# Kernel tuning notes

Hardware: AMD Instinct MI355X
Metric: run time of the kernel (lower is better)

The kernel has to match this reference:

```python
import jax, jax.numpy as jnp
import numpy as np

D_MODEL = 1024
D_K = 64  # d_model // heads


def setup_inputs() -> dict:
    key = jax.random.key(0)
    ks = jax.random.split(key, 9)
    B, S = 8, 2048
    q = jax.random.normal(ks[0], (B, S, D_MODEL), dtype=jnp.float32)
    k = jax.random.normal(ks[1], (B, S, D_MODEL), dtype=jnp.float32)
    v = jax.random.normal(ks[2], (B, S, D_MODEL), dtype=jnp.float32)
    # Causal mask: True = blocked (masked_fill with -inf)
    mask = ~jnp.tril(jnp.ones((S, S), dtype=bool))
    # Linear params (stored as [in, out]); torch Linear init ~ U(-1/sqrt(in), 1/sqrt(in))
    lim = 1.0 / np.sqrt(D_MODEL)
    Wq = jax.random.uniform(ks[3], (D_MODEL, D_K), jnp.float32, -lim, lim)
    Wk = jax.random.uniform(ks[4], (D_MODEL, D_K), jnp.float32, -lim, lim)
    Wv = jax.random.uniform(ks[5], (D_MODEL, D_K), jnp.float32, -lim, lim)
    bq = jax.random.uniform(ks[6], (D_K,), jnp.float32, -lim, lim)
    bk = jax.random.uniform(ks[7], (D_K,), jnp.float32, -lim, lim)
    bv = jax.random.uniform(ks[8], (D_K,), jnp.float32, -lim, lim)
    return {"q": q, "k": k, "v": v, "mask": mask,
            "Wq": Wq, "bq": bq, "Wk": Wk, "bk": bk, "Wv": Wv, "bv": bv}


def reference(q, k, v, mask, Wq, bq, Wk, bk, Wv, bv):
    qp = q @ Wq + bq              # [B, S, d_k]
    kp = k @ Wk + bk              # [B, S, d_k]
    vp = v @ Wv + bv              # [B, S, d_k]
    scale = 1.0 / jnp.sqrt(jnp.float32(D_K))
    scores = jnp.einsum("bqd,bkd->bqk", qp, kp) * scale  # [B, S, S]
    scores = jnp.where(mask, -jnp.inf, scores)
    attn = jax.nn.softmax(scores, axis=-1)
    return jnp.einsum("bqk,bkd->bqd", attn, vp)  # [B, S, d_k]
```

## Files before the change

### kernel.cpp

```cpp
#include <hip/hip_runtime.h>
#include <hip/hip_bf16.h>

typedef short s4 __attribute__((ext_vector_type(4)));
typedef short s8 __attribute__((ext_vector_type(8)));
typedef float f4 __attribute__((ext_vector_type(4)));

#define MFMA16(a, b, c) __builtin_amdgcn_mfma_f32_16x16x16bf16_1k(a, b, c, 0, 0, 0)

__device__ __forceinline__ short f2bf(float f) {
    union { float f; unsigned u; } v; v.f = f;
    unsigned r = v.u + 0x7fffu + ((v.u >> 16) & 1u);
    return (short)(r >> 16);
}

struct ProjArgs {
    const float* X[3];
    const float* W[3];
    const float* b[3];
    unsigned short* O[3];
};

__global__ __launch_bounds__(256) void proj_kernel(ProjArgs args) {
    __shared__ short lA[64][68];
    __shared__ short lW[64][68];

    const int t  = threadIdx.x;
    const int wv = t >> 6, ln = t & 63, lg = ln >> 4, lr = ln & 15;
    const int which = blockIdx.y;

    const float* X = args.X[which] + (size_t)blockIdx.x * 64 * 1024;
    const float* W = args.W[which];

    f4 acc[4] = {f4{0,0,0,0}, f4{0,0,0,0}, f4{0,0,0,0}, f4{0,0,0,0}};

    for (int kk = 0; kk < 1024; kk += 64) {
        #pragma unroll
        for (int i = 0; i < 4; ++i) {
            int f  = t + i * 256;
            int r  = f >> 4;
            int c4 = f & 15;
            f4 a = *(const f4*)(X + (size_t)r * 1024 + kk + c4 * 4);
            f4 w = *(const f4*)(W + (size_t)(kk + r) * 64 + c4 * 4);
            s4 ab; ab[0]=f2bf(a[0]); ab[1]=f2bf(a[1]); ab[2]=f2bf(a[2]); ab[3]=f2bf(a[3]);
            s4 wb; wb[0]=f2bf(w[0]); wb[1]=f2bf(w[1]); wb[2]=f2bf(w[2]); wb[3]=f2bf(w[3]);
            *(s4*)&lA[r][c4 * 4] = ab;
            *(s4*)&lW[r][c4 * 4] = wb;
        }
        __syncthreads();

        #pragma unroll
        for (int ks = 0; ks < 4; ++ks) {
            s4 af = *(const s4*)&lA[wv * 16 + lr][ks * 16 + 4 * lg];
            #pragma unroll
            for (int nf = 0; nf < 4; ++nf) {
                s4 bf;
                #pragma unroll
                for (int e = 0; e < 4; ++e)
                    bf[e] = lW[ks * 16 + 4 * lg + e][nf * 16 + lr];
                acc[nf] = MFMA16(af, bf, acc[nf]);
            }
        }
        __syncthreads();
    }

    const float* bias = args.b[which];
    unsigned short* O = args.O[which];
    #pragma unroll
    for (int nf = 0; nf < 4; ++nf) {
        float bs = bias[nf * 16 + lr];
        int col = nf * 16 + lr;
        #pragma unroll
        for (int e = 0; e < 4; ++e) {
            int r = wv * 16 + 4 * lg + e;
            int grow = blockIdx.x * 64 + r;
            unsigned short val = (unsigned short)f2bf(acc[nf][e] + bs);
            if (which == 2) {
                size_t idx = (size_t)(grow >> 11) * 131072
                           + (size_t)((grow & 2047) >> 6) * 4096
                           + (size_t)col * 64 + (grow & 63);
                O[idx] = val;
            } else {
                O[(size_t)grow * 64 + col] = val;
            }
        }
    }
}

__global__ __launch_bounds__(512) void attn_part(const unsigned short* __restrict__ qp,
                                                 const unsigned short* __restrict__ kp,
                                                 const unsigned short* __restrict__ vpT,
                                                 float* __restrict__ partO,
                                                 float* __restrict__ partML) {
    __shared__ short lK[2][2][64][72];
    __shared__ short lV[2][2][64][72];

    const int t    = threadIdx.x;
    const int wave = t >> 6, ln = t & 63, lg = ln >> 4, lr = ln & 15;
    const int half = wave >> 2, hw = wave & 3;
    const int b = blockIdx.y, x = blockIdx.x;
    const int qt = 31 - (x >> 1), z = x & 1;
    const int P = qt + 1;
    const int c = (P + 1) >> 1;
    const int base  = z ? c : 0;
    const int chunk = z ? (P - c) : c;
    const int hA = (chunk + 1) >> 1;
    const int qrow = qt * 64 + hw * 16 + lr;

    const int g = t >> 7, gi = t & 127, ghalf = g >> 1;
    const bool isV = (g & 1) != 0;
    const unsigned short* tb = (isV ? vpT : kp) + (size_t)b * 131072;

    const unsigned short* qpb = qp + (size_t)b * 131072;
    s4 qf[4];
    #pragma unroll
    for (int ks = 0; ks < 4; ++ks)
        qf[ks] = *(const s4*)(qpb + (size_t)qrow * 64 + ks * 16 + 4 * lg);

    f4 accO[4] = {f4{0,0,0,0}, f4{0,0,0,0}, f4{0,0,0,0}, f4{0,0,0,0}};
    float m = -3e38f, lsum = 0.f;

    s8 stg[4];
    {
        const unsigned short* p = tb + (size_t)(base + (ghalf ? hA : 0)) * 4096;
        #pragma unroll
        for (int i = 0; i < 4; ++i)
            stg[i] = *(const s8*)(p + (gi + 128 * i) * 8);
    }

    int buf = 0;
    for (int j = 0; j < hA; ++j) {
        {
            short (*dst)[72] = isV ? lV[ghalf][buf] : lK[ghalf][buf];
            #pragma unroll
            for (int i = 0; i < 4; ++i) {
                int s = gi + 128 * i;
                *(s8*)&dst[s >> 3][(s & 7) * 8] = stg[i];
            }
        }
        __syncthreads();

        if (j + 1 < hA) {
            const unsigned short* p = tb + (size_t)(base + (ghalf ? hA : 0) + j + 1) * 4096;
            #pragma unroll
            for (int i = 0; i < 4; ++i)
                stg[i] = *(const s8*)(p + (gi + 128 * i) * 8);
        }

        const int kt = base + (half ? hA : 0) + j;
        if (kt < base + chunk) {
            f4 st[4];
            #pragma unroll
            for (int kf = 0; kf < 4; ++kf) {
                f4 a = f4{0,0,0,0};
                #pragma unroll
                for (int ks = 0; ks < 4; ++ks) {
                    s4 kfr = *(const s4*)&lK[half][buf][kf * 16 + lr][ks * 16 + 4 * lg];
                    a = MFMA16(kfr, qf[ks], a);
                }
                st[kf] = a;
            }

            const bool diag = (kt == qt);
            const int kbase = kt * 64;
            float smax = -3e38f;
            #pragma unroll
            for (int kf = 0; kf < 4; ++kf) {
                #pragma unroll
                for (int e = 0; e < 4; ++e) {
                    float s = st[kf][e] * 0.125f;
                    if (diag && (kbase + kf * 16 + 4 * lg + e > qrow)) s = -3e38f;
                    st[kf][e] = s;
                    smax = fmaxf(smax, s);
                }
            }
            smax = fmaxf(smax, __shfl_xor(smax, 16));
            smax = fmaxf(smax, __shfl_xor(smax, 32));

            float mnew  = fmaxf(m, smax);
            float scale = __expf(m - mnew);
            float psum  = 0.f;
            s4 pf[4];
            #pragma unroll
            for (int kf = 0; kf < 4; ++kf) {
                f4 p;
                #pragma unroll
                for (int e = 0; e < 4; ++e) { p[e] = __expf(st[kf][e] - mnew); psum += p[e]; }
                s4 pb; pb[0]=f2bf(p[0]); pb[1]=f2bf(p[1]); pb[2]=f2bf(p[2]); pb[3]=f2bf(p[3]);
                pf[kf] = pb;
            }
            psum += __shfl_xor(psum, 16);
            psum += __shfl_xor(psum, 32);
            lsum = lsum * scale + psum;
            m = mnew;
            #pragma unroll
            for (int df = 0; df < 4; ++df) accO[df] *= scale;

            #pragma unroll
            for (int df = 0; df < 4; ++df) {
                #pragma unroll
                for (int kf = 0; kf < 4; ++kf) {
                    s4 vf = *(const s4*)&lV[half][buf][df * 16 + lr][kf * 16 + 4 * lg];
                    accO[df] = MFMA16(vf, pf[kf], accO[df]);
                }
            }
        }
        buf ^= 1;
    }

    __syncthreads();
    float* ex = (float*)&lK[0][0][0][0];
    const int idx = (hw * 64 + ln) * 19;
    if (half == 1) {
        ex[idx + 0] = m;
        ex[idx + 1] = lsum;
        #pragma unroll
        for (int df = 0; df < 4; ++df)
            #pragma unroll
            for (int e = 0; e < 4; ++e)
                ex[idx + 2 + df * 4 + e] = accO[df][e];
    }
    __syncthreads();
    if (half == 0) {
        float mB = ex[idx + 0], lB = ex[idx + 1];
        float mx = fmaxf(m, mB);
        float sA = __expf(m - mx), sB = __expf(mB - mx);
        float lP = lsum * sA + lB * sB;

        const size_t pidx = ((size_t)b * 32 + qt) * 2 + z;
        float* Od = partO + pidx * 4096;
        const int q = hw * 16 + lr;
        #pragma unroll
        for (int df = 0; df < 4; ++df) {
            f4 o;
            #pragma unroll
            for (int e = 0; e < 4; ++e)
                o[e] = accO[df][e] * sA + ex[idx + 2 + df * 4 + e] * sB;
            *(f4*)(Od + (size_t)q * 64 + df * 16 + 4 * lg) = o;
        }
        if (lg == 0) {
            partML[pidx * 128 + q * 2 + 0] = mx;
            partML[pidx * 128 + q * 2 + 1] = lP;
        }
    }
}

__global__ __launch_bounds__(256) void attn_merge(const float* __restrict__ partO,
                                                  const float* __restrict__ partML,
                                                  float* __restrict__ out) {
    const int t = threadIdx.x;
    const int g = blockIdx.x, b = blockIdx.y;
    const int q = t >> 2, dq = t & 3;

    const size_t p0 = ((size_t)b * 32 + g) * 2;
    const size_t p1 = p0 + 1;
    float m0 = partML[p0 * 128 + q * 2], l0 = partML[p0 * 128 + q * 2 + 1];
    float m1 = partML[p1 * 128 + q * 2], l1 = partML[p1 * 128 + q * 2 + 1];
    float M  = fmaxf(m0, m1);
    float s0 = __expf(m0 - M), s1 = __expf(m1 - M);
    float inv = 1.f / (l0 * s0 + l1 * s1);

    const float* O0 = partO + p0 * 4096 + (size_t)q * 64 + dq * 16;
    const float* O1 = partO + p1 * 4096 + (size_t)q * 64 + dq * 16;
    float* ob = out + ((size_t)b * 2048 + g * 64 + q) * 64 + dq * 16;
    #pragma unroll
    for (int i = 0; i < 4; ++i) {
        f4 a = *(const f4*)(O0 + 4 * i);
        f4 c = *(const f4*)(O1 + 4 * i);
        f4 o;
        #pragma unroll
        for (int e = 0; e < 4; ++e) o[e] = (a[e] * s0 + c[e] * s1) * inv;
        *(f4*)(ob + 4 * i) = o;
    }
}

extern "C" void kernel_launch(void* const* d_in, const int* in_sizes, int n_in,
                              void* d_out, int out_size, void* d_ws, size_t ws_size,
                              hipStream_t stream) {
    const float* q  = (const float*)d_in[0];
    const float* k  = (const float*)d_in[1];
    const float* v  = (const float*)d_in[2];
    const float* Wq = (const float*)d_in[4];
    const float* bq = (const float*)d_in[5];
    const float* Wk = (const float*)d_in[6];
    const float* bk = (const float*)d_in[7];
    const float* Wv = (const float*)d_in[8];
    const float* bv = (const float*)d_in[9];

    unsigned short* qp  = (unsigned short*)d_ws;
    unsigned short* kp  = qp + (size_t)16384 * 64;
    unsigned short* vpT = kp + (size_t)16384 * 64;
    float* partO  = (float*)(vpT + (size_t)16384 * 64);
    float* partML = partO + (size_t)512 * 4096;

    ProjArgs pa;
    pa.X[0] = q;  pa.X[1] = k;  pa.X[2] = v;
    pa.W[0] = Wq; pa.W[1] = Wk; pa.W[2] = Wv;
    pa.b[0] = bq; pa.b[1] = bk; pa.b[2] = bv;
    pa.O[0] = qp; pa.O[1] = kp; pa.O[2] = vpT;
    proj_kernel<<<dim3(256, 3), 256, 0, stream>>>(pa);

    attn_part<<<dim3(64, 8), 512, 0, stream>>>(qp, kp, vpT, partO, partML);
    attn_merge<<<dim3(32, 8), 256, 0, stream>>>(partO, partML, (float*)d_out);
}
```

Before: 78.67 us.

## Use 32x32 MFMA with 128-row query tiles and pre-convert weights to bf16

Restructures the attention kernel so each block handles 128 query rows: each wave owns 32 rows and uses the 32x32x8 bf16 MFMA, which cuts LDS re-reads of K/V per query and halves the grid. Masking now applies only to tiles that intersect the diagonal, and key tiles lying entirely above a wave's rows are skipped. A separate small kernel converts the projection weights to bf16 once, so the projection kernel loads bf16 directly instead of converting W in every block. The change adds a kernel launch, alters the LDS padding and the layout of the partial buffers, and halves the number of attention blocks, which may reduce occupancy across the GPU.

```diff
diff --git a/kernel.cpp b/kernel.cpp
--- a/kernel.cpp
+++ b/kernel.cpp
@@ -4,8 +4,10 @@
 typedef short s4 __attribute__((ext_vector_type(4)));
 typedef short s8 __attribute__((ext_vector_type(8)));
 typedef float f4 __attribute__((ext_vector_type(4)));
+typedef float f16v __attribute__((ext_vector_type(16)));
 
 #define MFMA16(a, b, c) __builtin_amdgcn_mfma_f32_16x16x16bf16_1k(a, b, c, 0, 0, 0)
+#define MFMA32(a, b, c) __builtin_amdgcn_mfma_f32_32x32x8bf16_1k(a, b, c, 0, 0, 0)
 
 __device__ __forceinline__ short f2bf(float f) {
     union { float f; unsigned u; } v; v.f = f;
@@ -13,23 +15,33 @@
     return (short)(r >> 16);
 }
 
+struct WcArgs { const float* W[3]; unsigned short* O; };
+
+__global__ __launch_bounds__(256) void wconv_kernel(WcArgs a) {
+    const int which = blockIdx.y;
+    const int id = blockIdx.x * 256 + threadIdx.x;
+    f4 w = *(const f4*)(a.W[which] + (size_t)id * 4);
+    s4 o; o[0]=f2bf(w[0]); o[1]=f2bf(w[1]); o[2]=f2bf(w[2]); o[3]=f2bf(w[3]);
+    *(s4*)(a.O + (size_t)which * 65536 + (size_t)id * 4) = o;
+}
+
 struct ProjArgs {
     const float* X[3];
-    const float* W[3];
     const float* b[3];
+    const unsigned short* Wbf;
     unsigned short* O[3];
 };
 
 __global__ __launch_bounds__(256) void proj_kernel(ProjArgs args) {
     __shared__ short lA[64][68];
-    __shared__ short lW[64][68];
+    __shared__ short lW[64][72];
 
     const int t  = threadIdx.x;
     const int wv = t >> 6, ln = t & 63, lg = ln >> 4, lr = ln & 15;
     const int which = blockIdx.y;
 
     const float* X = args.X[which] + (size_t)blockIdx.x * 64 * 1024;
-    const float* W = args.W[which];
+    const unsigned short* Wb = args.Wbf + (size_t)which * 65536;
 
     f4 acc[4] = {f4{0,0,0,0}, f4{0,0,0,0}, f4{0,0,0,0}, f4{0,0,0,0}};
 
@@ -40,11 +52,15 @@
             int r  = f >> 4;
             int c4 = f & 15;
             f4 a = *(const f4*)(X + (size_t)r * 1024 + kk + c4 * 4);
-            f4 w = *(const f4*)(W + (size_t)(kk + r) * 64 + c4 * 4);
             s4 ab; ab[0]=f2bf(a[0]); ab[1]=f2bf(a[1]); ab[2]=f2bf(a[2]); ab[3]=f2bf(a[3]);
-            s4 wb; wb[0]=f2bf(w[0]); wb[1]=f2bf(w[1]); wb[2]=f2bf(w[2]); wb[3]=f2bf(w[3]);
             *(s4*)&lA[r][c4 * 4] = ab;
-            *(s4*)&lW[r][c4 * 4] = wb;
+        }
+        #pragma unroll
+        for (int i = 0; i < 2; ++i) {
+            int s = t + i * 256;
+            int r = s >> 3, c8 = s & 7;
+            s8 w8 = *(const s8*)(Wb + (size_t)(kk + r) * 64 + c8 * 8);
+            *(s8*)&lW[r][c8 * 8] = w8;
         }
         __syncthreads();
 
@@ -91,37 +107,41 @@
                                                  const unsigned short* __restrict__ vpT,
                                                  float* __restrict__ partO,
                                                  float* __restrict__ partML) {
-    __shared__ short lK[2][2][64][72];
-    __shared__ short lV[2][2][64][72];
-
-    const int t    = threadIdx.x;
-    const int wave = t >> 6, ln = t & 63, lg = ln >> 4, lr = ln & 15;
-    const int half = wave >> 2, hw = wave & 3;
+    __shared__ short lK[2][2][64][76];
+    __shared__ short lV[2][2][64][76];
+
+    const int t = threadIdx.x;
+    const int wave = t >> 6, l = t & 63, lq = l & 31, h = l >> 5;
+    const int qcol = wave >> 1, half = wave & 1;
     const int b = blockIdx.y, x = blockIdx.x;
-    const int qt = 31 - (x >> 1), z = x & 1;
-    const int P = qt + 1;
-    const int c = (P + 1) >> 1;
-    const int base  = z ? c : 0;
-    const int chunk = z ? (P - c) : c;
-    const int hA = (chunk + 1) >> 1;
-    const int qrow = qt * 64 + hw * 16 + lr;
-
-    const int g = t >> 7, gi = t & 127, ghalf = g >> 1;
-    const bool isV = (g & 1) != 0;
-    const unsigned short* tb = (isV ? vpT : kp) + (size_t)b * 131072;
+    const int g = 15 - (x >> 1), z = x & 1;
+    const int cnt = g + 1;
+    const int base = z * cnt, hA = (cnt + 1) >> 1;
+    const int qg = 128 * g + 32 * qcol + lq;
+    const int qmaxw = 128 * g + 32 * qcol + 31;
+    const int qminw = 128 * g + 32 * qcol;
+
+    const int sg = t >> 7, gi = t & 127, sHalf = sg >> 1;
+    const bool sIsV = (sg & 1) != 0;
+    const unsigned short* tb = (sIsV ? vpT : kp) + (size_t)b * 131072;
 
     const unsigned short* qpb = qp + (size_t)b * 131072;
-    s4 qf[4];
+    s4 qf[8];
     #pragma unroll
-    for (int ks = 0; ks < 4; ++ks)
-        qf[ks] = *(const s4*)(qpb + (size_t)qrow * 64 + ks * 16 + 4 * lg);
-
-    f4 accO[4] = {f4{0,0,0,0}, f4{0,0,0,0}, f4{0,0,0,0}, f4{0,0,0,0}};
+    for (int ks = 0; ks < 8; ++ks)
+        qf[ks] = *(const s4*)(qpb + (size_t)qg * 64 + ks * 8 + 4 * h);
+
+    f16v accO[2];
+    #pragma unroll
+    for (int df = 0; df < 2; ++df)
+        #pragma unroll
+        for (int r = 0; r < 16; ++r) accO[df][r] = 0.f;
     float m = -3e38f, lsum = 0.f;
 
     s8 stg[4];
     {
-        const unsigned short* p = tb + (size_t)(base + (ghalf ? hA : 0)) * 4096;
+        int tile = base + (sHalf ? hA : 0); if (tile > 31) tile = 31;
+        const unsigned short* p = tb + (size_t)tile * 4096;
         #pragma unroll
         for (int i = 0; i < 4; ++i)
             stg[i] = *(const s8*)(p + (gi + 128 * i) * 8);
@@ -130,94 +150,105 @@
     int buf = 0;
     for (int j = 0; j < hA; ++j) {
         {
-            short (*dst)[72] = isV ? lV[ghalf][buf] : lK[ghalf][buf];
+            short (*dst)[76] = sIsV ? lV[sHalf][buf] : lK[sHalf][buf];
             #pragma unroll
             for (int i = 0; i < 4; ++i) {
                 int s = gi + 128 * i;
-                *(s8*)&dst[s >> 3][(s & 7) * 8] = stg[i];
+                s4 lo = __builtin_shufflevector(stg[i], stg[i], 0, 1, 2, 3);
+                s4 hi = __builtin_shufflevector(stg[i], stg[i], 4, 5, 6, 7);
+                *(s4*)&dst[s >> 3][(s & 7) * 8] = lo;
+                *(s4*)&dst[s >> 3][(s & 7) * 8 + 4] = hi;
             }
         }
         __syncthreads();
 
         if (j + 1 < hA) {
-            const unsigned short* p = tb + (size_t)(base + (ghalf ? hA : 0) + j + 1) * 4096;
+            int tile = base + (sHalf ? hA : 0) + j + 1; if (tile > 31) tile = 31;
+            const unsigned short* p = tb + (size_t)tile * 4096;
             #pragma unroll
             for (int i = 0; i < 4; ++i)
                 stg[i] = *(const s8*)(p + (gi + 128 * i) * 8);
         }
 
         const int kt = base + (half ? hA : 0) + j;
-        if (kt < base + chunk) {
-            f4 st[4];
-            #pragma unroll
-            for (int kf = 0; kf < 4; ++kf) {
-                f4 a = f4{0,0,0,0};
-                #pragma unroll
-                for (int ks = 0; ks < 4; ++ks) {
-                    s4 kfr = *(const s4*)&lK[half][buf][kf * 16 + lr][ks * 16 + 4 * lg];
-                    a = MFMA16(kfr, qf[ks], a);
+        const int kbase = kt * 64;
+        if (kt < base + cnt && kbase <= qmaxw) {
+            f16v st[2];
+            #pragma unroll
+            for (int s = 0; s < 2; ++s)
+                #pragma unroll
+                for (int r = 0; r < 16; ++r) st[s][r] = 0.f;
+            #pragma unroll
+            for (int ks = 0; ks < 8; ++ks) {
+                s4 k0 = *(const s4*)&lK[half][buf][lq][ks * 8 + 4 * h];
+                s4 k1 = *(const s4*)&lK[half][buf][32 + lq][ks * 8 + 4 * h];
+                st[0] = MFMA32(k0, qf[ks], st[0]);
+                st[1] = MFMA32(k1, qf[ks], st[1]);
+            }
+
+            const bool needMask = (kbase + 63 > qminw);
+            float smax = -3e38f;
+            #pragma unroll
+            for (int s = 0; s < 2; ++s)
+                #pragma unroll
+                for (int r = 0; r < 16; ++r) {
+                    int key = kbase + s * 32 + 8 * (r >> 2) + 4 * h + (r & 3);
+                    float val = st[s][r] * 0.125f;
+                    if (needMask && key > qg) val = -3e38f;
+                    st[s][r] = val;
+                    smax = fmaxf(smax, val);
                 }
-                st[kf] = a;
-            }
-
-            const bool diag = (kt == qt);
-            const int kbase = kt * 64;
-            float smax = -3e38f;
-            #pragma unroll
-            for (int kf = 0; kf < 4; ++kf) {
-                #pragma unroll
-                for (int e = 0; e < 4; ++e) {
-                    float s = st[kf][e] * 0.125f;
-                    if (diag && (kbase + kf * 16 + 4 * lg + e > qrow)) s = -3e38f;
-                    st[kf][e] = s;
-                    smax = fmaxf(smax, s);
-                }
-            }
-            smax = fmaxf(smax, __shfl_xor(smax, 16));
             smax = fmaxf(smax, __shfl_xor(smax, 32));
 
             float mnew  = fmaxf(m, smax);
             float scale = __expf(m - mnew);
-            float psum  = 0.f;
-            s4 pf[4];
-            #pragma unroll
-            for (int kf = 0; kf < 4; ++kf) {
-                f4 p;
-                #pragma unroll
-                for (int e = 0; e < 4; ++e) { p[e] = __expf(st[kf][e] - mnew); psum += p[e]; }
-                s4 pb; pb[0]=f2bf(p[0]); pb[1]=f2bf(p[1]); pb[2]=f2bf(p[2]); pb[3]=f2bf(p[3]);
-                pf[kf] = pb;
-            }
-            psum += __shfl_xor(psum, 16);
+            lsum *= scale;
+            m = mnew;
+            #pragma unroll
+            for (int df = 0; df < 2; ++df)
+                #pragma unroll
+                for (int r = 0; r < 16; ++r) accO[df][r] *= scale;
+
+            float psum = 0.f;
+            #pragma unroll
+            for (int s = 0; s < 2; ++s) {
+                s4 pf[4];
+                #pragma unroll
+                for (int ks = 0; ks < 4; ++ks) {
+                    f4 p;
+                    #pragma unroll
+                    for (int e = 0; e < 4; ++e)
+                        p[e] = __expf(st[s][4 * ks + e] - mnew);
+                    psum += (p[0] + p[1]) + (p[2] + p[3]);
+                    s4 pc; pc[0]=f2bf(p[0]); pc[1]=f2bf(p[1]); pc[2]=f2bf(p[2]); pc[3]=f2bf(p[3]);
+                    pf[ks] = pc;
+                }
+                #pragma unroll
+                for (int df = 0; df < 2; ++df)
+                    #pragma unroll
+                    for (int ks = 0; ks < 4; ++ks) {
+                        s4 vf = *(const s4*)&lV[half][buf][32 * df + lq]
+                                               [s * 32 + ks * 8 + 4 * h];
+                        accO[df] = MFMA32(vf, pf[ks], accO[df]);
+                    }
+            }
             psum += __shfl_xor(psum, 32);
-            lsum = lsum * scale + psum;
-            m = mnew;
-            #pragma unroll
-            for (int df = 0; df < 4; ++df) accO[df] *= scale;
-
-            #pragma unroll
-            for (int df = 0; df < 4; ++df) {
-                #pragma unroll
-                for (int kf = 0; kf < 4; ++kf) {
-                    s4 vf = *(const s4*)&lV[half][buf][df * 16 + lr][kf * 16 + 4 * lg];
-                    accO[df] = MFMA16(vf, pf[kf], accO[df]);
-                }
-            }
+            lsum += psum;
         }
         buf ^= 1;
     }
 
     __syncthreads();
     float* ex = (float*)&lK[0][0][0][0];
-    const int idx = (hw * 64 + ln) * 19;
+    const int idx = (qcol * 64 + l) * 34;
     if (half == 1) {
         ex[idx + 0] = m;
         ex[idx + 1] = lsum;
         #pragma unroll
-        for (int df = 0; df < 4; ++df)
-            #pragma unroll
-            for (int e = 0; e < 4; ++e)
-                ex[idx + 2 + df * 4 + e] = accO[df][e];
+        for (int df = 0; df < 2; ++df)
+            #pragma unroll
+            for (int r = 0; r < 16; ++r)
+                ex[idx + 2 + df * 16 + r] = accO[df][r];
     }
     __syncthreads();
     if (half == 0) {
@@ -226,20 +257,22 @@
         float sA = __expf(m - mx), sB = __expf(mB - mx);
         float lP = lsum * sA + lB * sB;
 
-        const size_t pidx = ((size_t)b * 32 + qt) * 2 + z;
-        float* Od = partO + pidx * 4096;
-        const int q = hw * 16 + lr;
-        #pragma unroll
-        for (int df = 0; df < 4; ++df) {
-            f4 o;
-            #pragma unroll
-            for (int e = 0; e < 4; ++e)
-                o[e] = accO[df][e] * sA + ex[idx + 2 + df * 4 + e] * sB;
-            *(f4*)(Od + (size_t)q * 64 + df * 16 + 4 * lg) = o;
-        }
-        if (lg == 0) {
-            partML[pidx * 128 + q * 2 + 0] = mx;
-            partML[pidx * 128 + q * 2 + 1] = lP;
+        const size_t pidx = ((size_t)(b * 16 + g)) * 2 + z;
+        float* Od = partO + pidx * 8192 + (size_t)(32 * qcol + lq) * 64;
+        #pragma unroll
+        for (int df = 0; df < 2; ++df)
+            #pragma unroll
+            for (int rg = 0; rg < 4; ++rg) {
+                f4 o;
+                #pragma unroll
+                for (int e = 0; e < 4; ++e)
+                    o[e] = accO[df][4 * rg + e] * sA
+                         + ex[idx + 2 + df * 16 + 4 * rg + e] * sB;
+                *(f4*)(Od + 32 * df + 8 * rg + 4 * h) = o;
+            }
+        if (h == 0) {
+            partML[pidx * 256 + (32 * qcol + lq) * 2 + 0] = mx;
+            partML[pidx * 256 + (32 * qcol + lq) * 2 + 1] = lP;
         }
     }
 }
@@ -248,22 +281,22 @@
                                                   const float* __restrict__ partML,
                                                   float* __restrict__ out) {
     const int t = threadIdx.x;
-    const int g = blockIdx.x, b = blockIdx.y;
-    const int q = t >> 2, dq = t & 3;
-
-    const size_t p0 = ((size_t)b * 32 + g) * 2;
+    const int gg = blockIdx.x, b = blockIdx.y;
+    const int q = t >> 1, dh = t & 1;
+
+    const size_t p0 = ((size_t)(b * 16 + gg)) * 2;
     const size_t p1 = p0 + 1;
-    float m0 = partML[p0 * 128 + q * 2], l0 = partML[p0 * 128 + q * 2 + 1];
-    float m1 = partML[p1 * 128 + q * 2], l1 = partML[p1 * 128 + q * 2 + 1];
+    float m0 = partML[p0 * 256 + q * 2], l0 = partML[p0 * 256 + q * 2 + 1];
+    float m1 = partML[p1 * 256 + q * 2], l1 = partML[p1 * 256 + q * 2 + 1];
     float M  = fmaxf(m0, m1);
     float s0 = __expf(m0 - M), s1 = __expf(m1 - M);
     float inv = 1.f / (l0 * s0 + l1 * s1);
 
-    const float* O0 = partO + p0 * 4096 + (size_t)q * 64 + dq * 16;
-    const float* O1 = partO + p1 * 4096 + (size_t)q * 64 + dq * 16;
-    float* ob = out + ((size_t)b * 2048 + g * 64 + q) * 64 + dq * 16;
+    const float* O0 = partO + p0 * 8192 + (size_t)q * 64 + dh * 32;
+    const float* O1 = partO + p1 * 8192 + (size_t)q * 64 + dh * 32;
+    float* ob = out + ((size_t)b * 2048 + gg * 128 + q) * 64 + dh * 32;
     #pragma unroll
-    for (int i = 0; i < 4; ++i) {
+    for (int i = 0; i < 8; ++i) {
         f4 a = *(const f4*)(O0 + 4 * i);
         f4 c = *(const f4*)(O1 + 4 * i);
         f4 o;
@@ -289,16 +322,22 @@
     unsigned short* qp  = (unsigned short*)d_ws;
     unsigned short* kp  = qp + (size_t)16384 * 64;
     unsigned short* vpT = kp + (size_t)16384 * 64;
-    float* partO  = (float*)(vpT + (size_t)16384 * 64);
-    float* partML = partO + (size_t)512 * 4096;
+    unsigned short* wbf = vpT + (size_t)16384 * 64;
+    float* partO  = (float*)(wbf + (size_t)3 * 65536);
+    float* partML = partO + (size_t)256 * 8192;
+
+    WcArgs wa;
+    wa.W[0] = Wq; wa.W[1] = Wk; wa.W[2] = Wv;
+    wa.O = wbf;
+    wconv_kernel<<<dim3(64, 3), 256, 0, stream>>>(wa);
 
     ProjArgs pa;
     pa.X[0] = q;  pa.X[1] = k;  pa.X[2] = v;
-    pa.W[0] = Wq; pa.W[1] = Wk; pa.W[2] = Wv;
     pa.b[0] = bq; pa.b[1] = bk; pa.b[2] = bv;
+    pa.Wbf = wbf;
     pa.O[0] = qp; pa.O[1] = kp; pa.O[2] = vpT;
     proj_kernel<<<dim3(256, 3), 256, 0, stream>>>(pa);
 
-    attn_part<<<dim3(64, 8), 512, 0, stream>>>(qp, kp, vpT, partO, partML);
-    attn_merge<<<dim3(32, 8), 256, 0, stream>>>(partO, partML, (float*)d_out);
-}
+    attn_part<<<dim3(32, 8), 512, 0, stream>>>(qp, kp, vpT, partO, partML);
+    attn_merge<<<dim3(16, 8), 256, 0, stream>>>(partO, partML, (float*)d_out);
+}
```

Result: slower. 88.31 us (+12.2%).
